# Optimization experiments

Measured on AMD Instinct MI355X. Metric: run time of the kernel, lower is better.

Reference implementation:

```python
import jax, jax.numpy as jnp
import numpy as np

SEQ, BATCH, HIDDEN, HEADS = 2048, 2, 1024, 16
HEAD_DIM = HIDDEN // HEADS
NORM = float(np.sqrt(HEAD_DIM))
NEG_MIN = float(np.finfo(np.float32).min)


def setup_inputs() -> dict:
    key = jax.random.key(0)
    ks = jax.random.split(key, 9)
    xavier = lambda k: (jax.random.normal(k, (HIDDEN, HIDDEN), jnp.float32)
                        * np.sqrt(2.0 / (HIDDEN + HIDDEN)))
    hidden_states = jax.random.normal(ks[0], (SEQ, BATCH, HIDDEN), jnp.float32)
    # causal (left-to-right) bool mask, True = attend
    attention_mask = jnp.tril(jnp.ones((SEQ, SEQ), dtype=bool))[None, None, :, :]
    return {
        "hidden_states": hidden_states,
        "attention_mask": attention_mask,
        "Wq": xavier(ks[1]), "bq": jnp.zeros((HIDDEN,), jnp.float32),
        "Wk": xavier(ks[2]), "bk": jnp.zeros((HIDDEN,), jnp.float32),
        "Wv": xavier(ks[3]), "bv": jnp.zeros((HIDDEN,), jnp.float32),
        "Wo": xavier(ks[4]), "bo": jnp.zeros((HIDDEN,), jnp.float32),
    }


def reference(hidden_states, attention_mask, Wq, bq, Wk, bk, Wv, bv, Wo, bo):
    s, b, _ = hidden_states.shape
    # projections (F.linear: x @ W.T + b), seq-first layout -> [s,b,h,d]
    q = (hidden_states @ Wq.T + bq).reshape(s, b, HEADS, HEAD_DIM) / NORM
    k = (hidden_states @ Wk.T + bk).reshape(s, b, HEADS, HEAD_DIM)
    v = (hidden_states @ Wv.T + bv).reshape(s, b, HEADS, HEAD_DIM)
    # scores [b,h,q,k] (Q already pre-scaled by 1/sqrt(d))
    scores = jnp.einsum("qbhd,kbhd->bhqk", q, k)
    scores = jnp.where(attention_mask, scores, NEG_MIN)
    probs = jax.nn.softmax(scores, axis=-1)
    # context [b,h,q,d] -> permute(2,0,1,3) -> [q,b,h,d] -> [q,b,hidden]
    ctx = jnp.einsum("bhqk,kbhd->qbhd", probs, v).reshape(s, b, HIDDEN)
    return ctx @ Wo.T + bo
```

## Files before the change

### kernel.cpp

```cpp
#include <hip/hip_runtime.h>
#include <hip/hip_bf16.h>
#include <cstdint>
#include <math.h>

#define SEQ 2048
#define BATCH 2
#define HID 1024
#define NH 16
#define HD 64
#define MROWS (SEQ * BATCH)

typedef __attribute__((ext_vector_type(8))) short bf16x8;
typedef __attribute__((ext_vector_type(4))) float f32x4;

typedef const __attribute__((address_space(1))) void* gas_t;
typedef __attribute__((address_space(3))) void* las_t;

static __device__ __forceinline__ unsigned short f2bf(float x) {
    __hip_bfloat16 h = __float2bfloat16(x);
    unsigned short u;
    __builtin_memcpy(&u, &h, 2);
    return u;
}

__global__ __launch_bounds__(256) void f2bf_kern(const float* __restrict__ in,
                                                 unsigned short* __restrict__ out,
                                                 int n8) {
    int i = blockIdx.x * 256 + threadIdx.x;
    if (i >= n8) return;
    const float4* p = (const float4*)in + (size_t)i * 2;
    float4 a = p[0], b = p[1];
    union { unsigned short us[8]; uint4 v; } o;
    o.us[0] = f2bf(a.x); o.us[1] = f2bf(a.y); o.us[2] = f2bf(a.z); o.us[3] = f2bf(a.w);
    o.us[4] = f2bf(b.x); o.us[5] = f2bf(b.y); o.us[6] = f2bf(b.z); o.us[7] = f2bf(b.w);
    ((uint4*)out)[i] = o.v;
}

#define GBK 32

__global__ __launch_bounds__(256) void gemm_bf16(const unsigned short* __restrict__ A,
                                                 const unsigned short* __restrict__ W,
                                                 const float* __restrict__ bias,
                                                 void* __restrict__ Cout,
                                                 float scale, int out_mode) {
    __shared__ unsigned short As[2][128 * GBK];
    __shared__ unsigned short Bs[2][128 * GBK];
    const int t = threadIdx.x;
    const int lane = t & 63, w = t >> 6;
    const int wr = w & 1, wc = w >> 1;
    const int m0 = blockIdx.x * 128, n0 = blockIdx.y * 128;

    f32x4 acc[4][4];
#pragma unroll
    for (int i = 0; i < 4; ++i)
#pragma unroll
        for (int j = 0; j < 4; ++j) acc[i][j] = {0.f, 0.f, 0.f, 0.f};

    const int srow = w * 16 + (lane >> 2);
    const int scol = (lane & 3) * 8;
    const unsigned short* gA = A + (size_t)(m0 + srow) * HID + scol;
    const unsigned short* gB = W + (size_t)(n0 + srow) * HID + scol;

    auto stage = [&](int buf, int k0) {
#pragma unroll
        for (int c = 0; c < 2; ++c) {
            __builtin_amdgcn_global_load_lds((gas_t)(gA + (size_t)c * 64 * HID + k0),
                                             (las_t)(&As[buf][(c * 64 + w * 16) * GBK]), 16, 0, 0);
            __builtin_amdgcn_global_load_lds((gas_t)(gB + (size_t)c * 64 * HID + k0),
                                             (las_t)(&Bs[buf][(c * 64 + w * 16) * GBK]), 16, 0, 0);
        }
    };

    const int arow = wr * 64 + (lane & 15);
    const int brow = wc * 64 + (lane & 15);
    const int kfo = (lane >> 4) * 8;

    stage(0, 0);
    int cur = 0;
    for (int k0 = 0; k0 < HID; k0 += GBK) {
        __syncthreads();
        if (k0 + GBK < HID) stage(cur ^ 1, k0 + GBK);
        bf16x8 af[4], bfr[4];
#pragma unroll
        for (int mt = 0; mt < 4; ++mt)
            af[mt] = *(const bf16x8*)(&As[cur][(arow + mt * 16) * GBK + kfo]);
#pragma unroll
        for (int nt = 0; nt < 4; ++nt)
            bfr[nt] = *(const bf16x8*)(&Bs[cur][(brow + nt * 16) * GBK + kfo]);
#pragma unroll
        for (int mt = 0; mt < 4; ++mt)
#pragma unroll
            for (int nt = 0; nt < 4; ++nt)
                acc[mt][nt] = __builtin_amdgcn_mfma_f32_16x16x32_bf16(
                    af[mt], bfr[nt], acc[mt][nt], 0, 0, 0);
        cur ^= 1;
    }

    float bvals[4];
#pragma unroll
    for (int nt = 0; nt < 4; ++nt)
        bvals[nt] = bias[n0 + wc * 64 + nt * 16 + (lane & 15)];

#pragma unroll
    for (int mt = 0; mt < 4; ++mt)
#pragma unroll
        for (int nt = 0; nt < 4; ++nt)
#pragma unroll
            for (int i = 0; i < 4; ++i) {
                float v = (acc[mt][nt][i] + bvals[nt]) * scale;
                int m = m0 + wr * 64 + mt * 16 + (lane >> 4) * 4 + i;
                int n = n0 + wc * 64 + nt * 16 + (lane & 15);
                if (out_mode == 0) {
                    ((unsigned short*)Cout)[(size_t)m * HID + n] = f2bf(v);
                } else if (out_mode == 1) {
                    ((unsigned short*)Cout)[(size_t)n * MROWS + (m & 1) * SEQ + (m >> 1)] = f2bf(v);
                } else {
                    ((float*)Cout)[(size_t)m * HID + n] = v;
                }
            }
}

__global__ __launch_bounds__(256) void attn_mfma(const unsigned short* __restrict__ Qb,
                                                 const unsigned short* __restrict__ Kb,
                                                 const unsigned short* __restrict__ Vt,
                                                 unsigned short* __restrict__ Ob) {
    __shared__ unsigned short Kl[2][64 * 64];
    __shared__ unsigned short Vl[2][64 * 64];
    __shared__ unsigned short QP[64 * 64];

    const int t = threadIdx.x;
    const int lane = t & 63, w = t >> 6;

    const int flat = (int)blockIdx.x + (int)blockIdx.y * 16;
    const int xcd = flat & 7, ii = flat >> 3;
    const int bh = xcd * 4 + (ii >> 4);
    const int p = ii & 15;
    const int b = bh >> 4, h = bh & 15;

    const int lrow_base = w * 8 + (lane >> 3);
    const int chunkb = (lane & 7) * 16;

    for (int pass = 0; pass < 2; ++pass) {
        const int qt = pass == 0 ? (31 - p) : p;
        const int q0 = qt * 64;
        if (pass) __syncthreads();

        auto stage_kv = [&](int buf, int kt) {
            const int k0 = kt * 64;
#pragma unroll
            for (int c = 0; c < 2; ++c) {
                int lr = c * 32 + lrow_base;
                int sb = chunkb ^ ((lr & 7) << 4);
                const unsigned short* ksrc =
                    Kb + ((size_t)(k0 + lr) * 2 + b) * HID + h * 64 + (sb >> 1);
                const unsigned short* vsrc =
                    Vt + (size_t)(h * 64 + lr) * MROWS + b * SEQ + k0 + (sb >> 1);
                __builtin_amdgcn_global_load_lds((gas_t)ksrc,
                    (las_t)(&Kl[buf][(c * 32 + w * 8) * 64]), 16, 0, 0);
                __builtin_amdgcn_global_load_lds((gas_t)vsrc,
                    (las_t)(&Vl[buf][(c * 32 + w * 8) * 64]), 16, 0, 0);
            }
        };

        stage_kv(0, 0);

#pragma unroll
        for (int c = 0; c < 2; ++c) {
            int f = c * 256 + t;
            int r = f >> 3, dc = f & 7;
            uint4 v = *(const uint4*)(Qb + (size_t)((q0 + r) * 2 + b) * HID + h * 64 + dc * 8);
            *(uint4*)((char*)QP + r * 128 + ((dc * 16) ^ ((r & 7) << 4))) = v;
        }

        f32x4 acc[4];
#pragma unroll
        for (int nt = 0; nt < 4; ++nt) acc[nt] = {0.f, 0.f, 0.f, 0.f};
        float mrow[4] = {-INFINITY, -INFINITY, -INFINITY, -INFINITY};
        float lrow[4] = {0.f, 0.f, 0.f, 0.f};
        bf16x8 qf[2];

        int cur = 0;
        for (int kt = 0; kt <= qt; ++kt) {
            __syncthreads();
            if (kt < qt) stage_kv(cur ^ 1, kt + 1);
            if (kt == 0) {
                int r = w * 16 + (lane & 15);
                int base = r * 128, sw = (r & 7) << 4;
                qf[0] = *(const bf16x8*)((char*)QP + base + ((((lane >> 4) * 16) + 0) ^ sw));
                qf[1] = *(const bf16x8*)((char*)QP + base + ((((lane >> 4) * 16) + 64) ^ sw));
            }
            const char* Kc = (const char*)Kl[cur];
            const char* Vc = (const char*)Vl[cur];

            f32x4 s[4];
#pragma unroll
            for (int ct = 0; ct < 4; ++ct) {
                int j = ct * 16 + (lane & 15);
                int base = j * 128, sw = (j & 7) << 4;
                bf16x8 kf0 = *(const bf16x8*)(Kc + base + ((((lane >> 4) * 16) + 0) ^ sw));
                bf16x8 kf1 = *(const bf16x8*)(Kc + base + ((((lane >> 4) * 16) + 64) ^ sw));
                f32x4 z = {0.f, 0.f, 0.f, 0.f};
                z = __builtin_amdgcn_mfma_f32_16x16x32_bf16(qf[0], kf0, z, 0, 0, 0);
                z = __builtin_amdgcn_mfma_f32_16x16x32_bf16(qf[1], kf1, z, 0, 0, 0);
                s[ct] = z;
            }

            if (kt == qt) {
#pragma unroll
                for (int ct = 0; ct < 4; ++ct) {
                    int j = ct * 16 + (lane & 15);
#pragma unroll
                    for (int i = 0; i < 4; ++i) {
                        int q = w * 16 + (lane >> 4) * 4 + i;
                        if (j > q) s[ct][i] = -3.0e38f;
                    }
                }
            }

#pragma unroll
            for (int i = 0; i < 4; ++i) {
                float mx = fmaxf(fmaxf(s[0][i], s[1][i]), fmaxf(s[2][i], s[3][i]));
                mx = fmaxf(mx, __shfl_xor(mx, 1));
                mx = fmaxf(mx, __shfl_xor(mx, 2));
                mx = fmaxf(mx, __shfl_xor(mx, 4));
                mx = fmaxf(mx, __shfl_xor(mx, 8));
                float mn = fmaxf(mrow[i], mx);
                float corr = __expf(mrow[i] - mn);
                mrow[i] = mn;
                float rs = 0.f;
#pragma unroll
                for (int ct = 0; ct < 4; ++ct) {
                    float pe = __expf(s[ct][i] - mn);
                    s[ct][i] = pe;
                    rs += pe;
                }
                rs += __shfl_xor(rs, 1);
                rs += __shfl_xor(rs, 2);
                rs += __shfl_xor(rs, 4);
                rs += __shfl_xor(rs, 8);
                lrow[i] = lrow[i] * corr + rs;
#pragma unroll
                for (int nt = 0; nt < 4; ++nt) acc[nt][i] *= corr;
            }

#pragma unroll
            for (int ct = 0; ct < 4; ++ct)
#pragma unroll
                for (int i = 0; i < 4; ++i) {
                    int r = w * 16 + (lane >> 4) * 4 + i;
                    int jb = (ct * 16 + (lane & 15)) * 2;
                    *(unsigned short*)((char*)QP + r * 128 + (jb ^ ((r & 7) << 4))) = f2bf(s[ct][i]);
                }
            asm volatile("s_waitcnt lgkmcnt(0)" ::: "memory");
            __builtin_amdgcn_sched_barrier(0);

            bf16x8 pf[2];
            {
                int r = w * 16 + (lane & 15);
                int base = r * 128, sw = (r & 7) << 4;
                pf[0] = *(const bf16x8*)((char*)QP + base + ((((lane >> 4) * 16) + 0) ^ sw));
                pf[1] = *(const bf16x8*)((char*)QP + base + ((((lane >> 4) * 16) + 64) ^ sw));
            }
#pragma unroll
            for (int nt = 0; nt < 4; ++nt) {
                int d = nt * 16 + (lane & 15);
                int base = d * 128, sw = (d & 7) << 4;
                bf16x8 v0 = *(const bf16x8*)(Vc + base + ((((lane >> 4) * 16) + 0) ^ sw));
                bf16x8 v1 = *(const bf16x8*)(Vc + base + ((((lane >> 4) * 16) + 64) ^ sw));
                acc[nt] = __builtin_amdgcn_mfma_f32_16x16x32_bf16(pf[0], v0, acc[nt], 0, 0, 0);
                acc[nt] = __builtin_amdgcn_mfma_f32_16x16x32_bf16(pf[1], v1, acc[nt], 0, 0, 0);
            }
            cur ^= 1;
        }

#pragma unroll
        for (int i = 0; i < 4; ++i) {
            float inv = 1.0f / lrow[i];
            int q = q0 + w * 16 + (lane >> 4) * 4 + i;
#pragma unroll
            for (int nt = 0; nt < 4; ++nt) {
                int col = h * 64 + nt * 16 + (lane & 15);
                Ob[(size_t)(q * 2 + b) * HID + col] = f2bf(acc[nt][i] * inv);
            }
        }
    }
}

extern "C" void kernel_launch(void* const* d_in, const int* in_sizes, int n_in,
                              void* d_out, int out_size, void* d_ws, size_t ws_size,
                              hipStream_t stream) {
    const float* hs = (const float*)d_in[0];
    const float* Wq = (const float*)d_in[2];
    const float* bq = (const float*)d_in[3];
    const float* Wk = (const float*)d_in[4];
    const float* bk = (const float*)d_in[5];
    const float* Wv = (const float*)d_in[6];
    const float* bv = (const float*)d_in[7];
    const float* Wo = (const float*)d_in[8];
    const float* bo = (const float*)d_in[9];

    char* ws = (char*)d_ws;
    unsigned short* hs_bf = (unsigned short*)(ws);
    unsigned short* Wq_bf = (unsigned short*)(ws + (8u << 20));
    unsigned short* Wk_bf = (unsigned short*)(ws + (10u << 20));
    unsigned short* Wv_bf = (unsigned short*)(ws + (12u << 20));
    unsigned short* Wo_bf = (unsigned short*)(ws + (14u << 20));
    unsigned short* Q_bf  = (unsigned short*)(ws + (16u << 20));
    unsigned short* K_bf  = (unsigned short*)(ws + (24u << 20));
    unsigned short* Vt_bf = (unsigned short*)(ws + (32u << 20));
    unsigned short* ctx_bf= (unsigned short*)(ws + (40u << 20));

    dim3 blk(256);
    hipLaunchKernelGGL(f2bf_kern, dim3(MROWS * HID / 8 / 256), blk, 0, stream, hs, hs_bf, MROWS * HID / 8);
    hipLaunchKernelGGL(f2bf_kern, dim3(HID * HID / 8 / 256), blk, 0, stream, Wq, Wq_bf, HID * HID / 8);
    hipLaunchKernelGGL(f2bf_kern, dim3(HID * HID / 8 / 256), blk, 0, stream, Wk, Wk_bf, HID * HID / 8);
    hipLaunchKernelGGL(f2bf_kern, dim3(HID * HID / 8 / 256), blk, 0, stream, Wv, Wv_bf, HID * HID / 8);
    hipLaunchKernelGGL(f2bf_kern, dim3(HID * HID / 8 / 256), blk, 0, stream, Wo, Wo_bf, HID * HID / 8);

    dim3 gg(MROWS / 128, HID / 128);
    hipLaunchKernelGGL(gemm_bf16, gg, blk, 0, stream, hs_bf, Wq_bf, bq, (void*)Q_bf, 0.125f, 0);
    hipLaunchKernelGGL(gemm_bf16, gg, blk, 0, stream, hs_bf, Wk_bf, bk, (void*)K_bf, 1.0f, 0);
    hipLaunchKernelGGL(gemm_bf16, gg, blk, 0, stream, hs_bf, Wv_bf, bv, (void*)Vt_bf, 1.0f, 1);

    hipLaunchKernelGGL(attn_mfma, dim3(16, 32), blk, 0, stream,
                       Q_bf, K_bf, Vt_bf, ctx_bf);

    hipLaunchKernelGGL(gemm_bf16, gg, blk, 0, stream, ctx_bf, Wo_bf, bo, d_out, 1.0f, 2);
}
```

Before: 291.7 us.

## Fuse Q/K/V projections into one GEMM launch and shrink M tile to 64

The three separate Q, K, V projection GEMMs become a single launch over a concatenated bf16 weight buffer, and each block picks bias, scale and output layout from its N segment. The GEMM tile drops from 128x128 to 64x128, with launch bounds set to allow 4 blocks per CU. This doubles the grid size for better CU occupancy and removes two launches. The cost is lower per-block data reuse and some extra per-element branching in the epilogue.

```diff
diff --git a/kernel.cpp b/kernel.cpp
--- a/kernel.cpp
+++ b/kernel.cpp
@@ -38,21 +38,22 @@
 
 #define GBK 32
 
-__global__ __launch_bounds__(256) void gemm_bf16(const unsigned short* __restrict__ A,
-                                                 const unsigned short* __restrict__ W,
-                                                 const float* __restrict__ bias,
-                                                 void* __restrict__ Cout,
-                                                 float scale, int out_mode) {
-    __shared__ unsigned short As[2][128 * GBK];
+__global__ __launch_bounds__(256, 4) void gemm_bf16(
+    const unsigned short* __restrict__ A, const unsigned short* __restrict__ W,
+    const float* __restrict__ b0, const float* __restrict__ b1,
+    const float* __restrict__ b2,
+    unsigned short* __restrict__ Qo, unsigned short* __restrict__ Ko,
+    unsigned short* __restrict__ Vo, float* __restrict__ Fo, int mode) {
+    __shared__ unsigned short As[2][64 * GBK];
     __shared__ unsigned short Bs[2][128 * GBK];
     const int t = threadIdx.x;
     const int lane = t & 63, w = t >> 6;
     const int wr = w & 1, wc = w >> 1;
-    const int m0 = blockIdx.x * 128, n0 = blockIdx.y * 128;
-
-    f32x4 acc[4][4];
-#pragma unroll
-    for (int i = 0; i < 4; ++i)
+    const int m0 = blockIdx.x * 64, n0 = blockIdx.y * 128;
+
+    f32x4 acc[2][4];
+#pragma unroll
+    for (int i = 0; i < 2; ++i)
 #pragma unroll
         for (int j = 0; j < 4; ++j) acc[i][j] = {0.f, 0.f, 0.f, 0.f};
 
@@ -62,16 +63,15 @@
     const unsigned short* gB = W + (size_t)(n0 + srow) * HID + scol;
 
     auto stage = [&](int buf, int k0) {
-#pragma unroll
-        for (int c = 0; c < 2; ++c) {
-            __builtin_amdgcn_global_load_lds((gas_t)(gA + (size_t)c * 64 * HID + k0),
-                                             (las_t)(&As[buf][(c * 64 + w * 16) * GBK]), 16, 0, 0);
+        __builtin_amdgcn_global_load_lds((gas_t)(gA + k0),
+                                         (las_t)(&As[buf][(w * 16) * GBK]), 16, 0, 0);
+#pragma unroll
+        for (int c = 0; c < 2; ++c)
             __builtin_amdgcn_global_load_lds((gas_t)(gB + (size_t)c * 64 * HID + k0),
                                              (las_t)(&Bs[buf][(c * 64 + w * 16) * GBK]), 16, 0, 0);
-        }
     };
 
-    const int arow = wr * 64 + (lane & 15);
+    const int arow = wr * 32 + (lane & 15);
     const int brow = wc * 64 + (lane & 15);
     const int kfo = (lane >> 4) * 8;
 
@@ -80,15 +80,15 @@
     for (int k0 = 0; k0 < HID; k0 += GBK) {
         __syncthreads();
         if (k0 + GBK < HID) stage(cur ^ 1, k0 + GBK);
-        bf16x8 af[4], bfr[4];
-#pragma unroll
-        for (int mt = 0; mt < 4; ++mt)
+        bf16x8 af[2], bfr[4];
+#pragma unroll
+        for (int mt = 0; mt < 2; ++mt)
             af[mt] = *(const bf16x8*)(&As[cur][(arow + mt * 16) * GBK + kfo]);
 #pragma unroll
         for (int nt = 0; nt < 4; ++nt)
             bfr[nt] = *(const bf16x8*)(&Bs[cur][(brow + nt * 16) * GBK + kfo]);
 #pragma unroll
-        for (int mt = 0; mt < 4; ++mt)
+        for (int mt = 0; mt < 2; ++mt)
 #pragma unroll
             for (int nt = 0; nt < 4; ++nt)
                 acc[mt][nt] = __builtin_amdgcn_mfma_f32_16x16x32_bf16(
@@ -96,26 +96,33 @@
         cur ^= 1;
     }
 
+    const int seg = n0 >> 10;
+    const float* bias = (mode == 1) ? b0 : (seg == 0 ? b0 : (seg == 1 ? b1 : b2));
+    const float scale = (mode == 0 && seg == 0) ? 0.125f : 1.0f;
+    const int nbase = (n0 & 1023) + wc * 64;
+
     float bvals[4];
 #pragma unroll
     for (int nt = 0; nt < 4; ++nt)
-        bvals[nt] = bias[n0 + wc * 64 + nt * 16 + (lane & 15)];
-
-#pragma unroll
-    for (int mt = 0; mt < 4; ++mt)
+        bvals[nt] = bias[nbase + nt * 16 + (lane & 15)];
+
+#pragma unroll
+    for (int mt = 0; mt < 2; ++mt)
 #pragma unroll
         for (int nt = 0; nt < 4; ++nt)
 #pragma unroll
             for (int i = 0; i < 4; ++i) {
                 float v = (acc[mt][nt][i] + bvals[nt]) * scale;
-                int m = m0 + wr * 64 + mt * 16 + (lane >> 4) * 4 + i;
-                int n = n0 + wc * 64 + nt * 16 + (lane & 15);
-                if (out_mode == 0) {
-                    ((unsigned short*)Cout)[(size_t)m * HID + n] = f2bf(v);
-                } else if (out_mode == 1) {
-                    ((unsigned short*)Cout)[(size_t)n * MROWS + (m & 1) * SEQ + (m >> 1)] = f2bf(v);
+                int m = m0 + wr * 32 + mt * 16 + (lane >> 4) * 4 + i;
+                int n = nbase + nt * 16 + (lane & 15);
+                if (mode == 1) {
+                    Fo[(size_t)m * HID + n] = v;
+                } else if (seg == 0) {
+                    Qo[(size_t)m * HID + n] = f2bf(v);
+                } else if (seg == 1) {
+                    Ko[(size_t)m * HID + n] = f2bf(v);
                 } else {
-                    ((float*)Cout)[(size_t)m * HID + n] = v;
+                    Vo[(size_t)n * MROWS + (m & 1) * SEQ + (m >> 1)] = f2bf(v);
                 }
             }
 }
@@ -300,30 +307,30 @@
     const float* bo = (const float*)d_in[9];
 
     char* ws = (char*)d_ws;
-    unsigned short* hs_bf = (unsigned short*)(ws);
-    unsigned short* Wq_bf = (unsigned short*)(ws + (8u << 20));
-    unsigned short* Wk_bf = (unsigned short*)(ws + (10u << 20));
-    unsigned short* Wv_bf = (unsigned short*)(ws + (12u << 20));
-    unsigned short* Wo_bf = (unsigned short*)(ws + (14u << 20));
-    unsigned short* Q_bf  = (unsigned short*)(ws + (16u << 20));
-    unsigned short* K_bf  = (unsigned short*)(ws + (24u << 20));
-    unsigned short* Vt_bf = (unsigned short*)(ws + (32u << 20));
-    unsigned short* ctx_bf= (unsigned short*)(ws + (40u << 20));
+    unsigned short* hs_bf   = (unsigned short*)(ws);
+    unsigned short* Wqkv_bf = (unsigned short*)(ws + (8u << 20));
+    unsigned short* Wo_bf   = (unsigned short*)(ws + (14u << 20));
+    unsigned short* Q_bf    = (unsigned short*)(ws + (16u << 20));
+    unsigned short* K_bf    = (unsigned short*)(ws + (24u << 20));
+    unsigned short* Vt_bf   = (unsigned short*)(ws + (32u << 20));
+    unsigned short* ctx_bf  = (unsigned short*)(ws + (40u << 20));
 
     dim3 blk(256);
+    const int WN8 = HID * HID / 8;
     hipLaunchKernelGGL(f2bf_kern, dim3(MROWS * HID / 8 / 256), blk, 0, stream, hs, hs_bf, MROWS * HID / 8);
-    hipLaunchKernelGGL(f2bf_kern, dim3(HID * HID / 8 / 256), blk, 0, stream, Wq, Wq_bf, HID * HID / 8);
-    hipLaunchKernelGGL(f2bf_kern, dim3(HID * HID / 8 / 256), blk, 0, stream, Wk, Wk_bf, HID * HID / 8);
-    hipLaunchKernelGGL(f2bf_kern, dim3(HID * HID / 8 / 256), blk, 0, stream, Wv, Wv_bf, HID * HID / 8);
-    hipLaunchKernelGGL(f2bf_kern, dim3(HID * HID / 8 / 256), blk, 0, stream, Wo, Wo_bf, HID * HID / 8);
-
-    dim3 gg(MROWS / 128, HID / 128);
-    hipLaunchKernelGGL(gemm_bf16, gg, blk, 0, stream, hs_bf, Wq_bf, bq, (void*)Q_bf, 0.125f, 0);
-    hipLaunchKernelGGL(gemm_bf16, gg, blk, 0, stream, hs_bf, Wk_bf, bk, (void*)K_bf, 1.0f, 0);
-    hipLaunchKernelGGL(gemm_bf16, gg, blk, 0, stream, hs_bf, Wv_bf, bv, (void*)Vt_bf, 1.0f, 1);
+    hipLaunchKernelGGL(f2bf_kern, dim3(WN8 / 256), blk, 0, stream, Wq, Wqkv_bf, WN8);
+    hipLaunchKernelGGL(f2bf_kern, dim3(WN8 / 256), blk, 0, stream, Wk, Wqkv_bf + (size_t)HID * HID, WN8);
+    hipLaunchKernelGGL(f2bf_kern, dim3(WN8 / 256), blk, 0, stream, Wv, Wqkv_bf + (size_t)2 * HID * HID, WN8);
+    hipLaunchKernelGGL(f2bf_kern, dim3(WN8 / 256), blk, 0, stream, Wo, Wo_bf, WN8);
+
+    hipLaunchKernelGGL(gemm_bf16, dim3(MROWS / 64, 24), blk, 0, stream,
+                       hs_bf, Wqkv_bf, bq, bk, bv, Q_bf, K_bf, Vt_bf, (float*)nullptr, 0);
 
     hipLaunchKernelGGL(attn_mfma, dim3(16, 32), blk, 0, stream,
                        Q_bf, K_bf, Vt_bf, ctx_bf);
 
-    hipLaunchKernelGGL(gemm_bf16, gg, blk, 0, stream, ctx_bf, Wo_bf, bo, d_out, 1.0f, 2);
-}
+    hipLaunchKernelGGL(gemm_bf16, dim3(MROWS / 64, 8), blk, 0, stream,
+                       ctx_bf, Wo_bf, bo, bo, bo,
+                       (unsigned short*)nullptr, (unsigned short*)nullptr,
+                       (unsigned short*)nullptr, (float*)d_out, 1);
+}
```

After: 245.7 us. -15.7%, faster.
